# Kernel optimization log

Measured on AMD Instinct MI355X. Metric: run time of the kernel, lower is better.

Reference implementation:

```python
import jax, jax.numpy as jnp
import numpy as np

B, N = 4096, 4096
BISECTION_ITERS = 40


def setup_inputs() -> dict:
    key = jax.random.key(0)
    kz, = jax.random.split(key, 1)
    z = jax.random.normal(kz, (B, N), dtype=jnp.float32)
    gamma = jnp.ones((N,), dtype=jnp.float32)   # GammaParam fixed, init=1, clamped at eps (no-op here)
    m = jnp.zeros((N,), dtype=jnp.float32)      # BoundsParam fixed, m_init=0
    M = jnp.ones((N,), dtype=jnp.float32)       # BoundsParam fixed, M_init=1
    xi = jnp.ones((B,), dtype=jnp.float32)      # fixed xi=1 expanded to batch
    return {"z": z, "gamma": gamma, "m": m, "M": M, "xi": xi}


def reference(z, gamma, m, M, xi):
    """Weighted L2 projection of z (B,N) onto {x: sum x = xi, m <= x <= M} via bisection on lambda."""
    Bq, Nq = z.shape
    gB = jnp.broadcast_to(gamma, (Bq, Nq))
    mB = jnp.broadcast_to(m, (Bq, Nq))
    MB = jnp.broadcast_to(M, (Bq, Nq))
    two_gamma = 2.0 * gB

    lam_low = jnp.min(two_gamma * (mB - z), axis=-1)   # (B,)
    lam_high = jnp.max(two_gamma * (MB - z), axis=-1)  # (B,)

    def body(_, carry):
        lo, hi = carry
        mid = 0.5 * (lo + hi)
        x_mid = jnp.clip(z + mid[:, None] / two_gamma, mB, MB)
        g_mid = jnp.sum(x_mid, axis=-1) - xi
        pos = g_mid > 0
        lo_new = jnp.where(pos, lo, mid)
        hi_new = jnp.where(pos, mid, hi)
        return (lo_new, hi_new)

    lam_low, lam_high = jax.lax.fori_loop(0, BISECTION_ITERS, body, (lam_low, lam_high))
    lam = 0.5 * (lam_low + lam_high)
    x = jnp.clip(z + lam[:, None] / two_gamma, mB, MB)
    return x
```

## Files before the change

kernel.cpp:

```cpp
#include <hip/hip_runtime.h>


#define BISECT_STEPS 6
#define TOTAL_STEPS  8

#define GLD_LDS16(gp, lp) __builtin_amdgcn_global_load_lds( \
    (const __attribute__((address_space(1))) void*)(gp),    \
    (__attribute__((address_space(3))) void*)(lp), 16, 0, 0)

template<int CTRL, int RM>
__device__ __forceinline__ float dpp_addf(float v) {
    int t = __builtin_amdgcn_update_dpp(0, __float_as_int(v), CTRL, RM, 0xf, false);
    return v + __int_as_float(t);
}
template<int CTRL, int RM>
__device__ __forceinline__ float dpp_minf(float v) {
    int t = __builtin_amdgcn_update_dpp(0x7f800000, __float_as_int(v), CTRL, RM, 0xf, false);
    return fminf(v, __int_as_float(t));
}
template<int CTRL, int RM>
__device__ __forceinline__ float dpp_maxf(float v) {
    int t = __builtin_amdgcn_update_dpp(0xff800000, __float_as_int(v), CTRL, RM, 0xf, false);
    return fmaxf(v, __int_as_float(t));
}
__device__ __forceinline__ float wave_sum(float v) {
    v = dpp_addf<0x111, 0xf>(v);
    v = dpp_addf<0x112, 0xf>(v);
    v = dpp_addf<0x114, 0xf>(v);
    v = dpp_addf<0x118, 0xf>(v);
    v = dpp_addf<0x142, 0xa>(v);
    v = dpp_addf<0x143, 0xc>(v);
    return __int_as_float(__builtin_amdgcn_readlane(__float_as_int(v), 63));
}
__device__ __forceinline__ float wave_min(float v) {
    v = dpp_minf<0x111, 0xf>(v);
    v = dpp_minf<0x112, 0xf>(v);
    v = dpp_minf<0x114, 0xf>(v);
    v = dpp_minf<0x118, 0xf>(v);
    v = dpp_minf<0x142, 0xa>(v);
    v = dpp_minf<0x143, 0xc>(v);
    return __int_as_float(__builtin_amdgcn_readlane(__float_as_int(v), 63));
}
__device__ __forceinline__ float wave_max(float v) {
    v = dpp_maxf<0x111, 0xf>(v);
    v = dpp_maxf<0x112, 0xf>(v);
    v = dpp_maxf<0x114, 0xf>(v);
    v = dpp_maxf<0x118, 0xf>(v);
    v = dpp_maxf<0x142, 0xa>(v);
    v = dpp_maxf<0x143, 0xc>(v);
    return __int_as_float(__builtin_amdgcn_readlane(__float_as_int(v), 63));
}

__device__ __forceinline__ float pick_cand(float lo, float hi, float glo,
                                           float ghi, int it) {
    const float w = hi - lo;
    if (it < BISECT_STEPS) return fmaf(0.5f, w, lo);
    const float denom = ghi - glo;
    float c = (lo * ghi - hi * glo) / denom;
    return fminf(fmaxf(c, fmaf(0.0625f, w, lo)), fmaf(-0.0625f, w, hi));
}

__global__ __launch_bounds__(256) void qp_proj2_n4096(
    const float* __restrict__ z,
    const float* __restrict__ gamma,
    const float* __restrict__ mlo,
    const float* __restrict__ mhi,
    const float* __restrict__ xi,
    float* __restrict__ out,
    int Btot)
{
    constexpr int N = 4096;
    const int tid  = threadIdx.x;
    const int lane = tid & 63;
    const int wid  = tid >> 6;
    const int rowA = blockIdx.x * 2;
    const int rowB = rowA + 1;
    const bool hasB = (rowB < Btot);

    __shared__ float4 zsB[N / 4];
    __shared__ float  red[4][4];
    __shared__ float  wsum[2][2][4];
    __shared__ int    uni[4];

    const float4* zA4 = reinterpret_cast<const float4*>(z + (size_t)rowA * N);
    const float4* g4  = reinterpret_cast<const float4*>(gamma);
    const float4* m4  = reinterpret_cast<const float4*>(mlo);
    const float4* M4  = reinterpret_cast<const float4*>(mhi);
    float4* oA4 = reinterpret_cast<float4*>(out + (size_t)rowA * N);
    float4* oB4 = reinterpret_cast<float4*>(out + (size_t)rowB * N);

    if (hasB) {
        const char* src = (const char*)(z + (size_t)rowB * N) + tid * 16;
        char* dst = (char*)zsB + tid * 16;
        #pragma unroll
        for (int k = 0; k < 4; ++k)
            GLD_LDS16(src + k * 4096, dst + k * 4096);
    }

    float za[16];
    float amn = INFINITY, amx = -INFINITY;
    #pragma unroll
    for (int k = 0; k < 4; ++k) {
        const float4 v = zA4[tid + k * 256];
        za[4*k+0] = v.x; za[4*k+1] = v.y; za[4*k+2] = v.z; za[4*k+3] = v.w;
        amn = fminf(amn, fminf(fminf(v.x, v.y), fminf(v.z, v.w)));
        amx = fmaxf(amx, fmaxf(fmaxf(v.x, v.y), fmaxf(v.z, v.w)));
    }
    amn = wave_min(amn);
    amx = wave_max(amx);

    const float g0 = gamma[0];
    const float m0 = mlo[0];
    const float M0 = mhi[0];
    bool oku = (g0 > 0.0f) && (M0 > m0);
    #pragma unroll
    for (int k = 0; k < 4; ++k) {
        const int idx = tid + k * 256;
        const float4 gg = g4[idx];
        const float4 mm = m4[idx];
        const float4 MM = M4[idx];
        oku = oku && (gg.x == g0) && (gg.y == g0) && (gg.z == g0) && (gg.w == g0)
                  && (mm.x == m0) && (mm.y == m0) && (mm.z == m0) && (mm.w == m0)
                  && (MM.x == M0) && (MM.y == M0) && (MM.z == M0) && (MM.w == M0);
    }
    if (lane == 0) uni[wid] = 0;
    const unsigned long long bal = __ballot(oku);

    const float xiA = xi[rowA];
    const float xiB = hasB ? xi[rowB] : 0.0f;

    asm volatile("s_waitcnt vmcnt(0)" ::: "memory");
    __builtin_amdgcn_sched_barrier(0);

    float bmn = INFINITY, bmx = -INFINITY;
    if (hasB) {
        #pragma unroll
        for (int k = 0; k < 4; ++k) {
            const float4 v = zsB[tid + k * 256];
            bmn = fminf(bmn, fminf(fminf(v.x, v.y), fminf(v.z, v.w)));
            bmx = fmaxf(bmx, fmaxf(fmaxf(v.x, v.y), fmaxf(v.z, v.w)));
        }
    } else {
        bmn = 0.0f; bmx = 0.0f;
    }
    bmn = wave_min(bmn);
    bmx = wave_max(bmx);
    if (lane == 0) {
        red[0][wid] = amn; red[1][wid] = amx;
        red[2][wid] = bmn; red[3][wid] = bmx;
        uni[wid] = (bal == 0xFFFFFFFFFFFFFFFFull) ? 1 : 0;
    }
    __syncthreads();
    const float zAmin = fminf(fminf(red[0][0], red[0][1]), fminf(red[0][2], red[0][3]));
    const float zAmax = fmaxf(fmaxf(red[1][0], red[1][1]), fmaxf(red[1][2], red[1][3]));
    const float zBmin = fminf(fminf(red[2][0], red[2][1]), fminf(red[2][2], red[2][3]));
    const float zBmax = fmaxf(fmaxf(red[3][0], red[3][1]), fmaxf(red[3][2], red[3][3]));
    const bool uniform = uni[0] && uni[1] && uni[2] && uni[3];

    if (uniform) {
        const float tg = 2.0f * g0;
        const float ia = 1.0f / tg;
        const float base_lo = (float)N * m0;
        const float base_hi = (float)N * M0;

        float loA = tg * (m0 - zAmax), hiA = tg * (M0 - zAmin);
        float gloA = base_lo - xiA,    ghiA = base_hi - xiA;
        int sideA = 0;
        float loB = tg * (m0 - zBmax), hiB = tg * (M0 - zBmin);
        float gloB = base_lo - xiB,    ghiB = base_hi - xiB;
        int sideB = 0;

        for (int it = 0; it < TOTAL_STEPS; ++it) {
            const float cA = pick_cand(loA, hiA, gloA, ghiA, it);
            const float cB = pick_cand(loB, hiB, gloB, ghiB, it);

            float a0 = 0.f, a1 = 0.f, a2 = 0.f, a3 = 0.f;
            #pragma unroll
            for (int q = 0; q < 4; ++q) {
                a0 += __builtin_amdgcn_fmed3f(fmaf(cA, ia, za[4*q+0]), m0, M0);
                a1 += __builtin_amdgcn_fmed3f(fmaf(cA, ia, za[4*q+1]), m0, M0);
                a2 += __builtin_amdgcn_fmed3f(fmaf(cA, ia, za[4*q+2]), m0, M0);
                a3 += __builtin_amdgcn_fmed3f(fmaf(cA, ia, za[4*q+3]), m0, M0);
            }
            float b0 = 0.f, b1 = 0.f, b2 = 0.f, b3 = 0.f;
            #pragma unroll
            for (int k = 0; k < 4; ++k) {
                const float4 v = zsB[tid + k * 256];
                b0 += __builtin_amdgcn_fmed3f(fmaf(cB, ia, v.x), m0, M0);
                b1 += __builtin_amdgcn_fmed3f(fmaf(cB, ia, v.y), m0, M0);
                b2 += __builtin_amdgcn_fmed3f(fmaf(cB, ia, v.z), m0, M0);
                b3 += __builtin_amdgcn_fmed3f(fmaf(cB, ia, v.w), m0, M0);
            }
            const float sA = wave_sum((a0 + a1) + (a2 + a3));
            const float sB = wave_sum((b0 + b1) + (b2 + b3));

            const int p = it & 1;
            if (lane == 0) { wsum[p][0][wid] = sA; wsum[p][1][wid] = sB; }
            __syncthreads();
            const float gA = ((wsum[p][0][0] + wsum[p][0][1]) + (wsum[p][0][2] + wsum[p][0][3])) - xiA;
            const float gB = ((wsum[p][1][0] + wsum[p][1][1]) + (wsum[p][1][2] + wsum[p][1][3])) - xiB;

            if (gA > 0.0f) { hiA = cA; if (sideA == 1) gloA *= 0.5f; ghiA = gA; sideA = 1; }
            else           { loA = cA; if (sideA == -1) ghiA *= 0.5f; gloA = gA; sideA = -1; }
            if (gB > 0.0f) { hiB = cB; if (sideB == 1) gloB *= 0.5f; ghiB = gB; sideB = 1; }
            else           { loB = cB; if (sideB == -1) ghiB *= 0.5f; gloB = gB; sideB = -1; }
        }

        const float dA = ghiA - gloA;
        float lamA = (dA > 0.0f) ? (loA * ghiA - hiA * gloA) / dA
                                 : fmaf(0.5f, hiA - loA, loA);
        lamA = fminf(fmaxf(lamA, loA), hiA);
        const float dB = ghiB - gloB;
        float lamB = (dB > 0.0f) ? (loB * ghiB - hiB * gloB) / dB
                                 : fmaf(0.5f, hiB - loB, loB);
        lamB = fminf(fmaxf(lamB, loB), hiB);

        #pragma unroll
        for (int k = 0; k < 4; ++k) {
            float4 r;
            r.x = __builtin_amdgcn_fmed3f(fmaf(lamA, ia, za[4*k+0]), m0, M0);
            r.y = __builtin_amdgcn_fmed3f(fmaf(lamA, ia, za[4*k+1]), m0, M0);
            r.z = __builtin_amdgcn_fmed3f(fmaf(lamA, ia, za[4*k+2]), m0, M0);
            r.w = __builtin_amdgcn_fmed3f(fmaf(lamA, ia, za[4*k+3]), m0, M0);
            oA4[tid + k * 256] = r;
        }
        if (hasB) {
            #pragma unroll
            for (int k = 0; k < 4; ++k) {
                const float4 v = zsB[tid + k * 256];
                float4 r;
                r.x = __builtin_amdgcn_fmed3f(fmaf(lamB, ia, v.x), m0, M0);
                r.y = __builtin_amdgcn_fmed3f(fmaf(lamB, ia, v.y), m0, M0);
                r.z = __builtin_amdgcn_fmed3f(fmaf(lamB, ia, v.z), m0, M0);
                r.w = __builtin_amdgcn_fmed3f(fmaf(lamB, ia, v.w), m0, M0);
                oB4[tid + k * 256] = r;
            }
        }
    } else {
        for (int rr = 0; rr < 2; ++rr) {
            const int row = rowA + rr;
            if (row >= Btot) break;
            const float4* zr = reinterpret_cast<const float4*>(z + (size_t)row * N);
            float4* orow = reinterpret_cast<float4*>(out + (size_t)row * N);
            const float xir = xi[row];

            float zb[16], ib[16], ma[16], Ma[16];
            float pmin = INFINITY, pmax = -INFINITY, psm = 0.0f, psM = 0.0f;
            #pragma unroll
            for (int k = 0; k < 4; ++k) {
                const int idx = tid + k * 256;
                const float4 zz = zr[idx];
                const float4 gg = g4[idx];
                const float4 mm = m4[idx];
                const float4 MM = M4[idx];
                const float zc[4] = {zz.x, zz.y, zz.z, zz.w};
                const float gc[4] = {gg.x, gg.y, gg.z, gg.w};
                const float mc[4] = {mm.x, mm.y, mm.z, mm.w};
                const float Mc[4] = {MM.x, MM.y, MM.z, MM.w};
                #pragma unroll
                for (int c = 0; c < 4; ++c) {
                    const int j = 4 * k + c;
                    const float tg2 = 2.0f * gc[c];
                    zb[j] = zc[c];
                    ib[j] = 1.0f / tg2;
                    ma[j] = mc[c];
                    Ma[j] = Mc[c];
                    pmin = fminf(pmin, tg2 * (mc[c] - zc[c]));
                    pmax = fmaxf(pmax, tg2 * (Mc[c] - zc[c]));
                    psm += mc[c];
                    psM += Mc[c];
                }
            }
            pmin = wave_min(pmin);
            pmax = wave_max(pmax);
            psm  = wave_sum(psm);
            psM  = wave_sum(psM);
            if (lane == 0) { red[0][wid] = pmin; red[1][wid] = pmax;
                             red[2][wid] = psm;  red[3][wid] = psM; }
            __syncthreads();
            float lo = fminf(fminf(red[0][0], red[0][1]), fminf(red[0][2], red[0][3]));
            float hi = fmaxf(fmaxf(red[1][0], red[1][1]), fmaxf(red[1][2], red[1][3]));
            float glo = ((red[2][0] + red[2][1]) + (red[2][2] + red[2][3])) - xir;
            float ghi = ((red[3][0] + red[3][1]) + (red[3][2] + red[3][3])) - xir;
            int side = 0;

            for (int it = 0; it < TOTAL_STEPS + 1; ++it) {
                const float cand = pick_cand(lo, hi, glo, ghi, it);
                float t0 = 0.f, t1 = 0.f, t2 = 0.f, t3 = 0.f;
                #pragma unroll
                for (int q = 0; q < 4; ++q) {
                    t0 += __builtin_amdgcn_fmed3f(fmaf(cand, ib[4*q+0], zb[4*q+0]), ma[4*q+0], Ma[4*q+0]);
                    t1 += __builtin_amdgcn_fmed3f(fmaf(cand, ib[4*q+1], zb[4*q+1]), ma[4*q+1], Ma[4*q+1]);
                    t2 += __builtin_amdgcn_fmed3f(fmaf(cand, ib[4*q+2], zb[4*q+2]), ma[4*q+2], Ma[4*q+2]);
                    t3 += __builtin_amdgcn_fmed3f(fmaf(cand, ib[4*q+3], zb[4*q+3]), ma[4*q+3], Ma[4*q+3]);
                }
                const float sw = wave_sum((t0 + t1) + (t2 + t3));
                const int p = it & 1;
                if (lane == 0) wsum[p][0][wid] = sw;
                __syncthreads();
                const float s = ((wsum[p][0][0] + wsum[p][0][1]) + (wsum[p][0][2] + wsum[p][0][3])) - xir;
                if (s > 0.0f) { hi = cand; if (side == 1) glo *= 0.5f; ghi = s; side = 1; }
                else          { lo = cand; if (side == -1) ghi *= 0.5f; glo = s; side = -1; }
            }

            const float denom = ghi - glo;
            float lam = (denom > 0.0f) ? (lo * ghi - hi * glo) / denom
                                       : fmaf(0.5f, hi - lo, lo);
            lam = fminf(fmaxf(lam, lo), hi);

            #pragma unroll
            for (int k = 0; k < 4; ++k) {
                float4 r;
                float xs[4];
                #pragma unroll
                for (int c = 0; c < 4; ++c) {
                    const int j = 4 * k + c;
                    xs[c] = __builtin_amdgcn_fmed3f(fmaf(lam, ib[j], zb[j]), ma[j], Ma[j]);
                }
                r.x = xs[0]; r.y = xs[1]; r.z = xs[2]; r.w = xs[3];
                orow[tid + k * 256] = r;
            }
            __syncthreads();
        }
    }
}

extern "C" void kernel_launch(void* const* d_in, const int* in_sizes, int n_in,
                              void* d_out, int out_size, void* d_ws, size_t ws_size,
                              hipStream_t stream) {
    const float* z     = (const float*)d_in[0];
    const float* gamma = (const float*)d_in[1];
    const float* m     = (const float*)d_in[2];
    const float* M     = (const float*)d_in[3];
    const float* xi    = (const float*)d_in[4];
    float* out = (float*)d_out;

    const int B = in_sizes[4];
    const int nblocks = (B + 1) / 2;
    qp_proj2_n4096<<<dim3(nblocks), dim3(256), 0, stream>>>(z, gamma, m, M, xi, out, B);
}
```

Measured before the change: 39.48 us.

## Remove uniform-parameter fast path and use general per-element gamma/bounds path

Drops the runtime check for uniform gamma/m/M and its scalar-constant fast path. It replaces the per-row fallback with a single general path that keeps the two-row-per-block structure. Each solver iteration now reloads gamma, m and M from global memory (cache) and recomputes the reciprocals per element, instead of using scalar constants. The gain is generality and a simpler kernel, at the cost of extra loads and divides inside the hot loop.

```diff
diff --git a/kernel.cpp b/kernel.cpp
--- a/kernel.cpp
+++ b/kernel.cpp
@@ -60,7 +60,7 @@
     return fminf(fmaxf(c, fmaf(0.0625f, w, lo)), fmaf(-0.0625f, w, hi));
 }
 
-__global__ __launch_bounds__(256) void qp_proj2_n4096(
+__global__ __launch_bounds__(256) void qp_proj2g_n4096(
     const float* __restrict__ z,
     const float* __restrict__ gamma,
     const float* __restrict__ mlo,
@@ -78,9 +78,8 @@
     const bool hasB = (rowB < Btot);
 
     __shared__ float4 zsB[N / 4];
-    __shared__ float  red[4][4];
+    __shared__ float  red[6][4];
     __shared__ float  wsum[2][2][4];
-    __shared__ int    uni[4];
 
     const float4* zA4 = reinterpret_cast<const float4*>(z + (size_t)rowA * N);
     const float4* g4  = reinterpret_cast<const float4*>(gamma);
@@ -98,229 +97,151 @@
     }
 
     float za[16];
-    float amn = INFINITY, amx = -INFINITY;
+    float pminA = INFINITY, pmaxA = -INFINITY;
+    float psm = 0.0f, psM = 0.0f;
     #pragma unroll
     for (int k = 0; k < 4; ++k) {
-        const float4 v = zA4[tid + k * 256];
+        const int idx = tid + k * 256;
+        const float4 v  = zA4[idx];
+        const float4 gg = g4[idx];
+        const float4 mm = m4[idx];
+        const float4 MM = M4[idx];
         za[4*k+0] = v.x; za[4*k+1] = v.y; za[4*k+2] = v.z; za[4*k+3] = v.w;
-        amn = fminf(amn, fminf(fminf(v.x, v.y), fminf(v.z, v.w)));
-        amx = fmaxf(amx, fmaxf(fmaxf(v.x, v.y), fmaxf(v.z, v.w)));
-    }
-    amn = wave_min(amn);
-    amx = wave_max(amx);
-
-    const float g0 = gamma[0];
-    const float m0 = mlo[0];
-    const float M0 = mhi[0];
-    bool oku = (g0 > 0.0f) && (M0 > m0);
+        const float zc[4] = {v.x, v.y, v.z, v.w};
+        const float gc[4] = {gg.x, gg.y, gg.z, gg.w};
+        const float mc[4] = {mm.x, mm.y, mm.z, mm.w};
+        const float Mc[4] = {MM.x, MM.y, MM.z, MM.w};
+        #pragma unroll
+        for (int c = 0; c < 4; ++c) {
+            const float tg = 2.0f * gc[c];
+            pminA = fminf(pminA, tg * (mc[c] - zc[c]));
+            pmaxA = fmaxf(pmaxA, tg * (Mc[c] - zc[c]));
+            psm += mc[c];
+            psM += Mc[c];
+        }
+    }
+
+    const float xiA = xi[rowA];
+    const float xiB = hasB ? xi[rowB] : 0.0f;
+
+    asm volatile("s_waitcnt vmcnt(0)" ::: "memory");
+    __builtin_amdgcn_sched_barrier(0);
+
+    float pminB = INFINITY, pmaxB = -INFINITY;
+    if (hasB) {
+        #pragma unroll
+        for (int k = 0; k < 4; ++k) {
+            const int idx = tid + k * 256;
+            const float4 v  = zsB[idx];
+            const float4 gg = g4[idx];
+            const float4 mm = m4[idx];
+            const float4 MM = M4[idx];
+            pminB = fminf(pminB, fminf(fminf(2.0f*gg.x*(mm.x - v.x), 2.0f*gg.y*(mm.y - v.y)),
+                                       fminf(2.0f*gg.z*(mm.z - v.z), 2.0f*gg.w*(mm.w - v.w))));
+            pmaxB = fmaxf(pmaxB, fmaxf(fmaxf(2.0f*gg.x*(MM.x - v.x), 2.0f*gg.y*(MM.y - v.y)),
+                                       fmaxf(2.0f*gg.z*(MM.z - v.z), 2.0f*gg.w*(MM.w - v.w))));
+        }
+    } else {
+        pminB = 0.0f; pmaxB = 1.0f;
+    }
+
+    pminA = wave_min(pminA);
+    pmaxA = wave_max(pmaxA);
+    pminB = wave_min(pminB);
+    pmaxB = wave_max(pmaxB);
+    psm   = wave_sum(psm);
+    psM   = wave_sum(psM);
+    if (lane == 0) {
+        red[0][wid] = pminA; red[1][wid] = pmaxA;
+        red[2][wid] = pminB; red[3][wid] = pmaxB;
+        red[4][wid] = psm;   red[5][wid] = psM;
+    }
+    __syncthreads();
+    float loA = fminf(fminf(red[0][0], red[0][1]), fminf(red[0][2], red[0][3]));
+    float hiA = fmaxf(fmaxf(red[1][0], red[1][1]), fmaxf(red[1][2], red[1][3]));
+    float loB = fminf(fminf(red[2][0], red[2][1]), fminf(red[2][2], red[2][3]));
+    float hiB = fmaxf(fmaxf(red[3][0], red[3][1]), fmaxf(red[3][2], red[3][3]));
+    const float smT = (red[4][0] + red[4][1]) + (red[4][2] + red[4][3]);
+    const float sMT = (red[5][0] + red[5][1]) + (red[5][2] + red[5][3]);
+
+    float gloA = smT - xiA, ghiA = sMT - xiA;
+    float gloB = smT - xiB, ghiB = sMT - xiB;
+    int sideA = 0, sideB = 0;
+
+    for (int it = 0; it < TOTAL_STEPS; ++it) {
+        const float cA = pick_cand(loA, hiA, gloA, ghiA, it);
+        const float cB = pick_cand(loB, hiB, gloB, ghiB, it);
+
+        float a0 = 0.f, a1 = 0.f, a2 = 0.f, a3 = 0.f;
+        float b0 = 0.f, b1 = 0.f, b2 = 0.f, b3 = 0.f;
+        #pragma unroll
+        for (int k = 0; k < 4; ++k) {
+            const int idx = tid + k * 256;
+            const float4 gg = g4[idx];
+            const float4 mm = m4[idx];
+            const float4 MM = M4[idx];
+            const float4 vb = zsB[idx];
+            const float i0 = 1.0f / (2.0f * gg.x);
+            const float i1 = 1.0f / (2.0f * gg.y);
+            const float i2 = 1.0f / (2.0f * gg.z);
+            const float i3 = 1.0f / (2.0f * gg.w);
+            a0 += __builtin_amdgcn_fmed3f(fmaf(cA, i0, za[4*k+0]), mm.x, MM.x);
+            a1 += __builtin_amdgcn_fmed3f(fmaf(cA, i1, za[4*k+1]), mm.y, MM.y);
+            a2 += __builtin_amdgcn_fmed3f(fmaf(cA, i2, za[4*k+2]), mm.z, MM.z);
+            a3 += __builtin_amdgcn_fmed3f(fmaf(cA, i3, za[4*k+3]), mm.w, MM.w);
+            b0 += __builtin_amdgcn_fmed3f(fmaf(cB, i0, vb.x), mm.x, MM.x);
+            b1 += __builtin_amdgcn_fmed3f(fmaf(cB, i1, vb.y), mm.y, MM.y);
+            b2 += __builtin_amdgcn_fmed3f(fmaf(cB, i2, vb.z), mm.z, MM.z);
+            b3 += __builtin_amdgcn_fmed3f(fmaf(cB, i3, vb.w), mm.w, MM.w);
+        }
+        const float sA = wave_sum((a0 + a1) + (a2 + a3));
+        const float sB = wave_sum((b0 + b1) + (b2 + b3));
+
+        const int p = it & 1;
+        if (lane == 0) { wsum[p][0][wid] = sA; wsum[p][1][wid] = sB; }
+        __syncthreads();
+        const float gA = ((wsum[p][0][0] + wsum[p][0][1]) + (wsum[p][0][2] + wsum[p][0][3])) - xiA;
+        const float gB = ((wsum[p][1][0] + wsum[p][1][1]) + (wsum[p][1][2] + wsum[p][1][3])) - xiB;
+
+        if (gA > 0.0f) { hiA = cA; if (sideA == 1) gloA *= 0.5f; ghiA = gA; sideA = 1; }
+        else           { loA = cA; if (sideA == -1) ghiA *= 0.5f; gloA = gA; sideA = -1; }
+        if (gB > 0.0f) { hiB = cB; if (sideB == 1) gloB *= 0.5f; ghiB = gB; sideB = 1; }
+        else           { loB = cB; if (sideB == -1) ghiB *= 0.5f; gloB = gB; sideB = -1; }
+    }
+
+    const float dA = ghiA - gloA;
+    float lamA = (dA > 0.0f) ? (loA * ghiA - hiA * gloA) / dA
+                             : fmaf(0.5f, hiA - loA, loA);
+    lamA = fminf(fmaxf(lamA, loA), hiA);
+    const float dB = ghiB - gloB;
+    float lamB = (dB > 0.0f) ? (loB * ghiB - hiB * gloB) / dB
+                             : fmaf(0.5f, hiB - loB, loB);
+    lamB = fminf(fmaxf(lamB, loB), hiB);
+
     #pragma unroll
     for (int k = 0; k < 4; ++k) {
         const int idx = tid + k * 256;
         const float4 gg = g4[idx];
         const float4 mm = m4[idx];
         const float4 MM = M4[idx];
-        oku = oku && (gg.x == g0) && (gg.y == g0) && (gg.z == g0) && (gg.w == g0)
-                  && (mm.x == m0) && (mm.y == m0) && (mm.z == m0) && (mm.w == m0)
-                  && (MM.x == M0) && (MM.y == M0) && (MM.z == M0) && (MM.w == M0);
-    }
-    if (lane == 0) uni[wid] = 0;
-    const unsigned long long bal = __ballot(oku);
-
-    const float xiA = xi[rowA];
-    const float xiB = hasB ? xi[rowB] : 0.0f;
-
-    asm volatile("s_waitcnt vmcnt(0)" ::: "memory");
-    __builtin_amdgcn_sched_barrier(0);
-
-    float bmn = INFINITY, bmx = -INFINITY;
-    if (hasB) {
-        #pragma unroll
-        for (int k = 0; k < 4; ++k) {
-            const float4 v = zsB[tid + k * 256];
-            bmn = fminf(bmn, fminf(fminf(v.x, v.y), fminf(v.z, v.w)));
-            bmx = fmaxf(bmx, fmaxf(fmaxf(v.x, v.y), fmaxf(v.z, v.w)));
-        }
-    } else {
-        bmn = 0.0f; bmx = 0.0f;
-    }
-    bmn = wave_min(bmn);
-    bmx = wave_max(bmx);
-    if (lane == 0) {
-        red[0][wid] = amn; red[1][wid] = amx;
-        red[2][wid] = bmn; red[3][wid] = bmx;
-        uni[wid] = (bal == 0xFFFFFFFFFFFFFFFFull) ? 1 : 0;
-    }
-    __syncthreads();
-    const float zAmin = fminf(fminf(red[0][0], red[0][1]), fminf(red[0][2], red[0][3]));
-    const float zAmax = fmaxf(fmaxf(red[1][0], red[1][1]), fmaxf(red[1][2], red[1][3]));
-    const float zBmin = fminf(fminf(red[2][0], red[2][1]), fminf(red[2][2], red[2][3]));
-    const float zBmax = fmaxf(fmaxf(red[3][0], red[3][1]), fmaxf(red[3][2], red[3][3]));
-    const bool uniform = uni[0] && uni[1] && uni[2] && uni[3];
-
-    if (uniform) {
-        const float tg = 2.0f * g0;
-        const float ia = 1.0f / tg;
-        const float base_lo = (float)N * m0;
-        const float base_hi = (float)N * M0;
-
-        float loA = tg * (m0 - zAmax), hiA = tg * (M0 - zAmin);
-        float gloA = base_lo - xiA,    ghiA = base_hi - xiA;
-        int sideA = 0;
-        float loB = tg * (m0 - zBmax), hiB = tg * (M0 - zBmin);
-        float gloB = base_lo - xiB,    ghiB = base_hi - xiB;
-        int sideB = 0;
-
-        for (int it = 0; it < TOTAL_STEPS; ++it) {
-            const float cA = pick_cand(loA, hiA, gloA, ghiA, it);
-            const float cB = pick_cand(loB, hiB, gloB, ghiB, it);
-
-            float a0 = 0.f, a1 = 0.f, a2 = 0.f, a3 = 0.f;
-            #pragma unroll
-            for (int q = 0; q < 4; ++q) {
-                a0 += __builtin_amdgcn_fmed3f(fmaf(cA, ia, za[4*q+0]), m0, M0);
-                a1 += __builtin_amdgcn_fmed3f(fmaf(cA, ia, za[4*q+1]), m0, M0);
-                a2 += __builtin_amdgcn_fmed3f(fmaf(cA, ia, za[4*q+2]), m0, M0);
-                a3 += __builtin_amdgcn_fmed3f(fmaf(cA, ia, za[4*q+3]), m0, M0);
-            }
-            float b0 = 0.f, b1 = 0.f, b2 = 0.f, b3 = 0.f;
-            #pragma unroll
-            for (int k = 0; k < 4; ++k) {
-                const float4 v = zsB[tid + k * 256];
-                b0 += __builtin_amdgcn_fmed3f(fmaf(cB, ia, v.x), m0, M0);
-                b1 += __builtin_amdgcn_fmed3f(fmaf(cB, ia, v.y), m0, M0);
-                b2 += __builtin_amdgcn_fmed3f(fmaf(cB, ia, v.z), m0, M0);
-                b3 += __builtin_amdgcn_fmed3f(fmaf(cB, ia, v.w), m0, M0);
-            }
-            const float sA = wave_sum((a0 + a1) + (a2 + a3));
-            const float sB = wave_sum((b0 + b1) + (b2 + b3));
-
-            const int p = it & 1;
-            if (lane == 0) { wsum[p][0][wid] = sA; wsum[p][1][wid] = sB; }
-            __syncthreads();
-            const float gA = ((wsum[p][0][0] + wsum[p][0][1]) + (wsum[p][0][2] + wsum[p][0][3])) - xiA;
-            const float gB = ((wsum[p][1][0] + wsum[p][1][1]) + (wsum[p][1][2] + wsum[p][1][3])) - xiB;
-
-            if (gA > 0.0f) { hiA = cA; if (sideA == 1) gloA *= 0.5f; ghiA = gA; sideA = 1; }
-            else           { loA = cA; if (sideA == -1) ghiA *= 0.5f; gloA = gA; sideA = -1; }
-            if (gB > 0.0f) { hiB = cB; if (sideB == 1) gloB *= 0.5f; ghiB = gB; sideB = 1; }
-            else           { loB = cB; if (sideB == -1) ghiB *= 0.5f; gloB = gB; sideB = -1; }
-        }
-
-        const float dA = ghiA - gloA;
-        float lamA = (dA > 0.0f) ? (loA * ghiA - hiA * gloA) / dA
-                                 : fmaf(0.5f, hiA - loA, loA);
-        lamA = fminf(fmaxf(lamA, loA), hiA);
-        const float dB = ghiB - gloB;
-        float lamB = (dB > 0.0f) ? (loB * ghiB - hiB * gloB) / dB
-                                 : fmaf(0.5f, hiB - loB, loB);
-        lamB = fminf(fmaxf(lamB, loB), hiB);
-
-        #pragma unroll
-        for (int k = 0; k < 4; ++k) {
-            float4 r;
-            r.x = __builtin_amdgcn_fmed3f(fmaf(lamA, ia, za[4*k+0]), m0, M0);
-            r.y = __builtin_amdgcn_fmed3f(fmaf(lamA, ia, za[4*k+1]), m0, M0);
-            r.z = __builtin_amdgcn_fmed3f(fmaf(lamA, ia, za[4*k+2]), m0, M0);
-            r.w = __builtin_amdgcn_fmed3f(fmaf(lamA, ia, za[4*k+3]), m0, M0);
-            oA4[tid + k * 256] = r;
-        }
+        const float i0 = 1.0f / (2.0f * gg.x);
+        const float i1 = 1.0f / (2.0f * gg.y);
+        const float i2 = 1.0f / (2.0f * gg.z);
+        const float i3 = 1.0f / (2.0f * gg.w);
+        float4 ra;
+        ra.x = __builtin_amdgcn_fmed3f(fmaf(lamA, i0, za[4*k+0]), mm.x, MM.x);
+        ra.y = __builtin_amdgcn_fmed3f(fmaf(lamA, i1, za[4*k+1]), mm.y, MM.y);
+        ra.z = __builtin_amdgcn_fmed3f(fmaf(lamA, i2, za[4*k+2]), mm.z, MM.z);
+        ra.w = __builtin_amdgcn_fmed3f(fmaf(lamA, i3, za[4*k+3]), mm.w, MM.w);
+        oA4[idx] = ra;
         if (hasB) {
-            #pragma unroll
-            for (int k = 0; k < 4; ++k) {
-                const float4 v = zsB[tid + k * 256];
-                float4 r;
-                r.x = __builtin_amdgcn_fmed3f(fmaf(lamB, ia, v.x), m0, M0);
-                r.y = __builtin_amdgcn_fmed3f(fmaf(lamB, ia, v.y), m0, M0);
-                r.z = __builtin_amdgcn_fmed3f(fmaf(lamB, ia, v.z), m0, M0);
-                r.w = __builtin_amdgcn_fmed3f(fmaf(lamB, ia, v.w), m0, M0);
-                oB4[tid + k * 256] = r;
-            }
-        }
-    } else {
-        for (int rr = 0; rr < 2; ++rr) {
-            const int row = rowA + rr;
-            if (row >= Btot) break;
-            const float4* zr = reinterpret_cast<const float4*>(z + (size_t)row * N);
-            float4* orow = reinterpret_cast<float4*>(out + (size_t)row * N);
-            const float xir = xi[row];
-
-            float zb[16], ib[16], ma[16], Ma[16];
-            float pmin = INFINITY, pmax = -INFINITY, psm = 0.0f, psM = 0.0f;
-            #pragma unroll
-            for (int k = 0; k < 4; ++k) {
-                const int idx = tid + k * 256;
-                const float4 zz = zr[idx];
-                const float4 gg = g4[idx];
-                const float4 mm = m4[idx];
-                const float4 MM = M4[idx];
-                const float zc[4] = {zz.x, zz.y, zz.z, zz.w};
-                const float gc[4] = {gg.x, gg.y, gg.z, gg.w};
-                const float mc[4] = {mm.x, mm.y, mm.z, mm.w};
-                const float Mc[4] = {MM.x, MM.y, MM.z, MM.w};
-                #pragma unroll
-                for (int c = 0; c < 4; ++c) {
-                    const int j = 4 * k + c;
-                    const float tg2 = 2.0f * gc[c];
-                    zb[j] = zc[c];
-                    ib[j] = 1.0f / tg2;
-                    ma[j] = mc[c];
-                    Ma[j] = Mc[c];
-                    pmin = fminf(pmin, tg2 * (mc[c] - zc[c]));
-                    pmax = fmaxf(pmax, tg2 * (Mc[c] - zc[c]));
-                    psm += mc[c];
-                    psM += Mc[c];
-                }
-            }
-            pmin = wave_min(pmin);
-            pmax = wave_max(pmax);
-            psm  = wave_sum(psm);
-            psM  = wave_sum(psM);
-            if (lane == 0) { red[0][wid] = pmin; red[1][wid] = pmax;
-                             red[2][wid] = psm;  red[3][wid] = psM; }
-            __syncthreads();
-            float lo = fminf(fminf(red[0][0], red[0][1]), fminf(red[0][2], red[0][3]));
-            float hi = fmaxf(fmaxf(red[1][0], red[1][1]), fmaxf(red[1][2], red[1][3]));
-            float glo = ((red[2][0] + red[2][1]) + (red[2][2] + red[2][3])) - xir;
-            float ghi = ((red[3][0] + red[3][1]) + (red[3][2] + red[3][3])) - xir;
-            int side = 0;
-
-            for (int it = 0; it < TOTAL_STEPS + 1; ++it) {
-                const float cand = pick_cand(lo, hi, glo, ghi, it);
-                float t0 = 0.f, t1 = 0.f, t2 = 0.f, t3 = 0.f;
-                #pragma unroll
-                for (int q = 0; q < 4; ++q) {
-                    t0 += __builtin_amdgcn_fmed3f(fmaf(cand, ib[4*q+0], zb[4*q+0]), ma[4*q+0], Ma[4*q+0]);
-                    t1 += __builtin_amdgcn_fmed3f(fmaf(cand, ib[4*q+1], zb[4*q+1]), ma[4*q+1], Ma[4*q+1]);
-                    t2 += __builtin_amdgcn_fmed3f(fmaf(cand, ib[4*q+2], zb[4*q+2]), ma[4*q+2], Ma[4*q+2]);
-                    t3 += __builtin_amdgcn_fmed3f(fmaf(cand, ib[4*q+3], zb[4*q+3]), ma[4*q+3], Ma[4*q+3]);
-                }
-                const float sw = wave_sum((t0 + t1) + (t2 + t3));
-                const int p = it & 1;
-                if (lane == 0) wsum[p][0][wid] = sw;
-                __syncthreads();
-                const float s = ((wsum[p][0][0] + wsum[p][0][1]) + (wsum[p][0][2] + wsum[p][0][3])) - xir;
-                if (s > 0.0f) { hi = cand; if (side == 1) glo *= 0.5f; ghi = s; side = 1; }
-                else          { lo = cand; if (side == -1) ghi *= 0.5f; glo = s; side = -1; }
-            }
-
-            const float denom = ghi - glo;
-            float lam = (denom > 0.0f) ? (lo * ghi - hi * glo) / denom
-                                       : fmaf(0.5f, hi - lo, lo);
-            lam = fminf(fmaxf(lam, lo), hi);
-
-            #pragma unroll
-            for (int k = 0; k < 4; ++k) {
-                float4 r;
-                float xs[4];
-                #pragma unroll
-                for (int c = 0; c < 4; ++c) {
-                    const int j = 4 * k + c;
-                    xs[c] = __builtin_amdgcn_fmed3f(fmaf(lam, ib[j], zb[j]), ma[j], Ma[j]);
-                }
-                r.x = xs[0]; r.y = xs[1]; r.z = xs[2]; r.w = xs[3];
-                orow[tid + k * 256] = r;
-            }
-            __syncthreads();
+            const float4 vb = zsB[idx];
+            float4 rb;
+            rb.x = __builtin_amdgcn_fmed3f(fmaf(lamB, i0, vb.x), mm.x, MM.x);
+            rb.y = __builtin_amdgcn_fmed3f(fmaf(lamB, i1, vb.y), mm.y, MM.y);
+            rb.z = __builtin_amdgcn_fmed3f(fmaf(lamB, i2, vb.z), mm.z, MM.z);
+            rb.w = __builtin_amdgcn_fmed3f(fmaf(lamB, i3, vb.w), mm.w, MM.w);
+            oB4[idx] = rb;
         }
     }
 }
@@ -337,5 +258,5 @@
 
     const int B = in_sizes[4];
     const int nblocks = (B + 1) / 2;
-    qp_proj2_n4096<<<dim3(nblocks), dim3(256), 0, stream>>>(z, gamma, m, M, xi, out, B);
-}
+    qp_proj2g_n4096<<<dim3(nblocks), dim3(256), 0, stream>>>(z, gamma, m, M, xi, out, B);
+}
```

Result: slower. 40.65 us (+3.0%).
